# Optimization experiments

Measured on AMD Instinct MI355X. Metric: run time of the kernel, lower is better.

Reference implementation:

```python
import jax, jax.numpy as jnp
import numpy as np
from jax import lax

FACTOR = 2
FIR = (1.0, 3.0, 3.0, 1.0)


def _fir_kernel():
    k1 = jnp.array(FIR, dtype=jnp.float32)
    k = jnp.outer(k1, k1)
    k = k / jnp.sum(k)
    return k * (FACTOR ** 2)  # gain=1, factor=2 -> x4


def _upfirdn2d(x, kernel, up, down, pad):
    # x: [N, C, H, W]; kernel: [kh, kw]; faithful to upfirdn2d_native:
    # upsample by zero-insertion (lhs_dilation), pad, convolve with flipped
    # kernel (F.conv2d is correlation of flipped kernel == true convolution),
    # then downsample by striding. lax.conv_general_dilated is correlation,
    # so pass the flipped kernel.
    C = x.shape[1]
    kflip = kernel[::-1, ::-1]
    w = jnp.tile(kflip[None, None], (C, 1, 1, 1))  # depthwise [C,1,kh,kw]
    return lax.conv_general_dilated(
        x, w,
        window_strides=(down, down),
        padding=[(pad[0], pad[1]), (pad[0], pad[1])],
        lhs_dilation=(up, up),
        feature_group_count=C,
        dimension_numbers=("NCHW", "OIHW", "NCHW"),
    )


def setup_inputs() -> dict:
    key = jax.random.key(0)
    k1, k2, k3 = jax.random.split(key, 3)
    N, C, H, W = 8, 256, 64, 64
    outC = 256
    hidden_states = jax.random.normal(k1, (N, C, H, W), dtype=jnp.float32)
    weight = jax.random.normal(k2, (outC, C, 3, 3), dtype=jnp.float32) * 0.05
    bias = jax.random.normal(k3, (outC,), dtype=jnp.float32)
    return {"hidden_states": hidden_states, "weight": weight, "bias": bias}


def reference(hidden_states, weight, bias):
    # FirUpsample2D.forward with use_conv=True, fir_kernel=(1,3,3,1), factor=2.
    k = _fir_kernel()  # [4, 4]
    convH, convW = weight.shape[2], weight.shape[3]
    pad_value = k.shape[0] - FACTOR - (convW - 1)  # = 0 here

    # The torch code flips+channel-swaps the weight then calls conv_transpose2d
    # (which itself flips and channel-swaps); the two cancel, so the net op is
    # plain cross-correlation of the ORIGINAL weight over the factor-dilated
    # input with (kH-1) padding on each side (output_padding == 0).
    x = lax.conv_general_dilated(
        hidden_states, weight,
        window_strides=(1, 1),
        padding=[(convH - 1, convH - 1), (convW - 1, convW - 1)],
        lhs_dilation=(FACTOR, FACTOR),
        dimension_numbers=("NCHW", "OIHW", "NCHW"),
    )  # [N, outC, (H-1)*2+3, (W-1)*2+3]

    out = _upfirdn2d(
        x, k, up=1, down=1,
        pad=((pad_value + 1) // 2 + FACTOR - 1, pad_value // 2 + 1),
    )  # [N, outC, 2H, 2W]

    return out + bias[None, :, None, None]
```

## Files before the change

### kernel.cpp

```cpp
#include <hip/hip_runtime.h>
#include <cstdint>
#include <cstddef>

typedef _Float16 f16;
typedef _Float16 f16x8 __attribute__((ext_vector_type(8)));
typedef float f32x4 __attribute__((ext_vector_type(4)));

#define AS1 __attribute__((address_space(1)))
#define AS3 __attribute__((address_space(3)))

__device__ __forceinline__ void gl_lds16(const void* g, void* l) {
  __builtin_amdgcn_global_load_lds((AS1 void*)g, (AS3 void*)l, 16u, 0, 0u);
}

__constant__ float c_tab[2][3][3] = {
  {{0.75f, 0.25f, 0.00f}, {0.25f, 0.75f, 0.75f}, {0.00f, 0.00f, 0.25f}},
  {{0.25f, 0.00f, 0.00f}, {0.75f, 0.75f, 0.25f}, {0.00f, 0.25f, 0.75f}}
};

__global__ __launch_bounds__(256) void prep_k(const float* __restrict__ W,
                                              const float* __restrict__ In,
                                              f16* __restrict__ Et,
                                              f16* __restrict__ Ah) {
  const int b = blockIdx.x;
  const int tid = threadIdx.x;
  if (b < 256) {
    const int oc = b;
    const int ic = tid;
    const int c = ic >> 5, icl = ic & 31;
    float w[9];
    const float* wp = W + ((size_t)oc * 256 + ic) * 9;
#pragma unroll
    for (int t = 0; t < 9; ++t) w[t] = wp[t];
#pragma unroll
    for (int py = 0; py < 2; ++py)
#pragma unroll
      for (int px = 0; px < 2; ++px) {
        const int jj = oc * 4 + py * 2 + px;
#pragma unroll
        for (int ay = 0; ay < 3; ++ay)
#pragma unroll
          for (int ax = 0; ax < 3; ++ax) {
            float s = 0.f;
#pragma unroll
            for (int iy = 0; iy < 3; ++iy)
#pragma unroll
              for (int ix = 0; ix < 3; ++ix)
                s += w[iy * 3 + ix] * c_tab[py][ay][iy] * c_tab[px][ax][ix];
            Et[((size_t)(((c * 3 + ay) * 3 + ax) * 1024 + jj)) * 32 + icl] = (f16)s;
          }
      }
  } else {
    const int bid2 = b - 256;
    const int icc = bid2 & 7;
    const int v = bid2 >> 3;
    const int n = v / 66;
    const int yp = v - n * 66;
    const int ic0 = icc * 32;
    const int icl = tid & 31, x8 = tid >> 5;
    f16* rowbase = Ah + ((size_t)(n * 66 + yp) * 66) * 256 + ic0;
    if (yp == 0 || yp == 65) {
#pragma unroll
      for (int i = 0; i < 9; ++i) {
        const int xp = i * 8 + x8;
        if (xp < 66) rowbase[(size_t)xp * 256 + icl] = (f16)0.f;
      }
    } else {
      const int y = yp - 1;
      __shared__ float tile[32][65];
      const int xl = tid & 63, icl4 = tid >> 6;
      const float* src = In + (((size_t)(n * 256 + ic0)) * 64 + y) * 64;
#pragma unroll
      for (int i = 0; i < 8; ++i) {
        const int icl_ = i * 4 + icl4;
        tile[icl_][xl] = src[(size_t)icl_ * 4096 + xl];
      }
      __syncthreads();
      f16* dst = rowbase + 256;
#pragma unroll
      for (int i = 0; i < 8; ++i) {
        const int x = i * 8 + x8;
        dst[(size_t)x * 256 + icl] = (f16)tile[icl][x];
      }
      if (x8 == 0) {
        rowbase[icl] = (f16)0.f;
        rowbase[(size_t)65 * 256 + icl] = (f16)0.f;
      }
    }
  }
}

__global__ __launch_bounds__(256) void gemm_k(const f16* __restrict__ Ah,
                                              const f16* __restrict__ Et,
                                              const float* __restrict__ bias,
                                              float* __restrict__ out) {
  __shared__ __align__(256) f16 lA[2][4224];
  __shared__ __align__(256) f16 lB[2][12288];
  const int tid = threadIdx.x;
  const int wave = tid >> 6;
  const int lane = tid & 63;
  const int bid = blockIdx.x;
  const int nt = bid & 7;
  const int mt = bid >> 3;
  const int m0 = mt * 128;
  const int jj0 = nt * 128;
  const int n = m0 >> 12;
  const int y0 = (m0 >> 6) & 63;

  const int hig = (lane & 3) ^ ((lane >> 3) & 3);
  int goA[2];
#pragma unroll
  for (int i = 0; i < 2; ++i) {
    const int s = wave * 2 + i;
    const int u = s * 16 + (lane >> 2);
    const int row = (u >= 66) ? 1 : 0;
    const int x = u - 66 * row;
    goA[i] = ((row * 66 + x) * 256 + hig * 8) * 2;
  }
  const int goAt = ((66 + 62 + wave) * 256 + (((lane ^ (wave >> 1)) & 3)) * 8) * 2;
  int goB[6];
#pragma unroll
  for (int j = 0; j < 6; ++j) {
    const int t = wave + 4 * j;
    const int ax = t >> 3, sub = t & 7;
    goB[j] = (ax * 32768 + (sub * 16 + (lane >> 2)) * 32 + hig * 8) * 2;
  }
  char* const lAb = (char*)lA;
  char* const lBb = (char*)lB;

  const int wm = wave >> 1, wn = wave & 1;
  const int lr = lane & 15;
  const int hi16 = (lane >> 4) * 16;
  int rdA[4][3];
#pragma unroll
  for (int mi = 0; mi < 4; ++mi)
#pragma unroll
    for (int ax = 0; ax < 3; ++ax) {
      const int o = wm * 4224 + (lr + mi * 16 + ax) * 64 + hi16;
      rdA[mi][ax] = o ^ (((o >> 7) & 3) << 4);
    }
  int rdB[4][3];
#pragma unroll
  for (int ni = 0; ni < 4; ++ni)
#pragma unroll
    for (int ax = 0; ax < 3; ++ax) {
      const int o = (wn * 64 + lr) * 64 + hi16 + ax * 8192 + ni * 1024;
      rdB[ni][ax] = o ^ (((o >> 7) & 3) << 4);
    }

  const char* const aN = (const char*)Ah + (size_t)(n * 66 + y0) * 33792;
  const char* const bE = (const char*)Et + (size_t)jj0 * 64;

  const f32x4 vzero = {0.f, 0.f, 0.f, 0.f};
  f32x4 acc[4][4];
#pragma unroll
  for (int i = 0; i < 4; ++i)
#pragma unroll
    for (int j = 0; j < 4; ++j) acc[i][j] = vzero;

  {
    gl_lds16(aN + goA[0], lAb + (wave * 2 + 0) * 1024);
    gl_lds16(aN + goA[1], lAb + (wave * 2 + 1) * 1024);
    if (lane < 4) gl_lds16(aN + goAt, lAb + 8192 + wave * 64);
#pragma unroll
    for (int j = 0; j < 6; ++j) gl_lds16(bE + goB[j], lBb + (wave + 4 * j) * 1024);
  }

  const char* aPn = aN + 33792;
  const char* bPn = bE + 196608;
  int ayn = 1;

#pragma unroll 1
  for (int t = 0; t < 24; ++t) {
    const int p = t & 1;

    if (t < 23) {
      char* dA = lAb + (p ^ 1) * 8448;
      char* dB = lBb + (p ^ 1) * 24576;
      gl_lds16(aPn + goA[0], dA + (wave * 2 + 0) * 1024);
      gl_lds16(aPn + goA[1], dA + (wave * 2 + 1) * 1024);
      if (lane < 4) gl_lds16(aPn + goAt, dA + 8192 + wave * 64);
#pragma unroll
      for (int j = 0; j < 6; ++j) gl_lds16(bPn + goB[j], dB + (wave + 4 * j) * 1024);
      bPn += 196608;
      if (ayn == 2) { aPn -= 67520; ayn = 0; }
      else          { aPn += 33792; ++ayn; }
      asm volatile("s_waitcnt vmcnt(9)" ::: "memory");
    } else {
      asm volatile("s_waitcnt vmcnt(0)" ::: "memory");
    }
    __builtin_amdgcn_s_barrier();
    __builtin_amdgcn_sched_barrier(0);

    const char* sA = lAb + p * 8448;
    const char* sB = lBb + p * 24576;
    f16x8 af[3][4], bf[3][4];
#pragma unroll
    for (int ax = 0; ax < 3; ++ax) {
#pragma unroll
      for (int mi = 0; mi < 4; ++mi) af[ax][mi] = *(const f16x8*)(sA + rdA[mi][ax]);
#pragma unroll
      for (int ni = 0; ni < 4; ++ni) bf[ax][ni] = *(const f16x8*)(sB + rdB[ni][ax]);
    }
    asm volatile("s_waitcnt lgkmcnt(0)" ::: "memory");
    __builtin_amdgcn_sched_barrier(0);
    __builtin_amdgcn_s_barrier();

#pragma unroll
    for (int ax = 0; ax < 3; ++ax)
#pragma unroll
      for (int mi = 0; mi < 4; ++mi)
#pragma unroll
        for (int ni = 0; ni < 4; ++ni)
          acc[mi][ni] = __builtin_amdgcn_mfma_f32_16x16x32_f16(af[ax][mi], bf[ax][ni],
                                                               acc[mi][ni], 0, 0, 0);
  }

  const int yw = y0 + wm;
#pragma unroll
  for (int ni = 0; ni < 4; ++ni) {
    const int jj = jj0 + wn * 64 + ni * 16 + lr;
    const int oc = jj >> 2;
    const int py = (jj >> 1) & 1, px = jj & 1;
    const float bv = bias[oc];
    const int oy = 2 * yw + py;
    float* orow = out + ((size_t)(n * 256 + oc) * 128 + oy) * 128;
#pragma unroll
    for (int mi = 0; mi < 4; ++mi) {
      const int xb = mi * 16 + ((lane >> 4) << 2);
#pragma unroll
      for (int v = 0; v < 4; ++v) {
        orow[2 * (xb + v) + px] = acc[mi][ni][v] + bv;
      }
    }
  }
}

__global__ __launch_bounds__(256) void fallback_k(const float* __restrict__ In,
                                                  const float* __restrict__ W,
                                                  const float* __restrict__ bias,
                                                  float* __restrict__ out) {
  const size_t idx = (size_t)blockIdx.x * 256 + threadIdx.x;
  const int ox = (int)(idx & 127), oy = (int)((idx >> 7) & 127);
  const int oc = (int)((idx >> 14) & 255);
  const int n = (int)(idx >> 22);
  const int px = ox & 1, py = oy & 1;
  const int x = ox >> 1, y = oy >> 1;
  float cy[3][3], cx[3][3];
#pragma unroll
  for (int a = 0; a < 3; ++a)
#pragma unroll
    for (int i = 0; i < 3; ++i) {
      cy[a][i] = c_tab[py][a][i];
      cx[a][i] = c_tab[px][a][i];
    }
  float acc = 0.f;
  const float* wbase = W + (size_t)oc * 2304;
  for (int ic = 0; ic < 256; ++ic) {
    const float* ib = In + (((size_t)(n * 256 + ic)) * 64 + y) * 64 + x;
    float pin[3][3];
#pragma unroll
    for (int ay = 0; ay < 3; ++ay) {
      const int yy = y + ay - 1;
#pragma unroll
      for (int ax = 0; ax < 3; ++ax) {
        const int xx = x + ax - 1;
        pin[ay][ax] = (yy >= 0 && yy < 64 && xx >= 0 && xx < 64)
                          ? ib[(ay - 1) * 64 + (ax - 1)] : 0.f;
      }
    }
    const float* w = wbase + ic * 9;
    float U[3][3];
#pragma unroll
    for (int ay = 0; ay < 3; ++ay)
#pragma unroll
      for (int ix = 0; ix < 3; ++ix)
        U[ay][ix] = cx[0][ix] * pin[ay][0] + cx[1][ix] * pin[ay][1] + cx[2][ix] * pin[ay][2];
#pragma unroll
    for (int iy = 0; iy < 3; ++iy)
#pragma unroll
      for (int ix = 0; ix < 3; ++ix) {
        const float V = cy[0][iy] * U[0][ix] + cy[1][iy] * U[1][ix] + cy[2][iy] * U[2][ix];
        acc += w[iy * 3 + ix] * V;
      }
  }
  out[idx] = acc + bias[oc];
}

extern "C" void kernel_launch(void* const* d_in, const int* in_sizes, int n_in,
                              void* d_out, int out_size, void* d_ws, size_t ws_size,
                              hipStream_t stream) {
  const float* In = (const float*)d_in[0];
  const float* W = (const float*)d_in[1];
  const float* bias = (const float*)d_in[2];
  float* out = (float*)d_out;

  const size_t E_BYTES = (size_t)1024 * 2304 * 2;
  const size_t A_BYTES = (size_t)8 * 66 * 66 * 256 * 2;

  if (ws_size >= E_BYTES + A_BYTES) {
    f16* Et = (f16*)d_ws;
    f16* Ah = (f16*)((char*)d_ws + E_BYTES);
    prep_k<<<256 + 4224, 256, 0, stream>>>(W, In, Et, Ah);
    gemm_k<<<2048, 256, 0, stream>>>(Ah, Et, bias, out);
  } else {
    fallback_k<<<131072, 256, 0, stream>>>(In, W, bias, out);
  }
}
```

Baseline: 337.7 us.

## Enlarge GEMM tile to 256x256 with 512 threads and interleaved prefetch

Restructures the implicit-GEMM kernel from 128x128 tiles with 4 waves to 256x256 tiles with 8 waves, doubling LDS buffers and per-wave accumulators (8x4 MFMA tiles). The global-to-LDS prefetch for the next K-step is now issued inside the first ax sub-step, and LDS fragment loads are split per ax and interleaved with MFMA under raised wave priority. Block indices are remapped so consecutive blocks share the same M rows across N tiles, improving L2 reuse. The larger tile increases arithmetic intensity but raises register and LDS pressure (about 100KB LDS per block) and adds more barriers per iteration.

```diff
diff --git a/kernel.cpp b/kernel.cpp
--- a/kernel.cpp
+++ b/kernel.cpp
@@ -90,20 +90,20 @@
   }
 }
 
-__global__ __launch_bounds__(256) void gemm_k(const f16* __restrict__ Ah,
-                                              const f16* __restrict__ Et,
-                                              const float* __restrict__ bias,
-                                              float* __restrict__ out) {
-  __shared__ __align__(256) f16 lA[2][4224];
-  __shared__ __align__(256) f16 lB[2][12288];
+__global__ __launch_bounds__(512, 2) void gemm_k(const f16* __restrict__ Ah,
+                                                 const f16* __restrict__ Et,
+                                                 const float* __restrict__ bias,
+                                                 float* __restrict__ out) {
+  __shared__ __align__(256) f16 lA[2][8448];
+  __shared__ __align__(256) f16 lB[2][24576];
   const int tid = threadIdx.x;
   const int wave = tid >> 6;
   const int lane = tid & 63;
-  const int bid = blockIdx.x;
-  const int nt = bid & 7;
-  const int mt = bid >> 3;
-  const int m0 = mt * 128;
-  const int jj0 = nt * 128;
+  const int bid = (blockIdx.x & 7) * 64 + (blockIdx.x >> 3);
+  const int nt = bid & 3;
+  const int mt = bid >> 2;
+  const int m0 = mt * 256;
+  const int jj0 = nt * 256;
   const int n = m0 >> 12;
   const int y0 = (m0 >> 6) & 63;
 
@@ -113,121 +113,121 @@
   for (int i = 0; i < 2; ++i) {
     const int s = wave * 2 + i;
     const int u = s * 16 + (lane >> 2);
-    const int row = (u >= 66) ? 1 : 0;
-    const int x = u - 66 * row;
-    goA[i] = ((row * 66 + x) * 256 + hig * 8) * 2;
-  }
-  const int goAt = ((66 + 62 + wave) * 256 + (((lane ^ (wave >> 1)) & 3)) * 8) * 2;
+    const int r = u / 66;
+    const int xi = u - r * 66;
+    goA[i] = r * 33792 + xi * 512 + hig * 16;
+  }
+  const int goAt = 3 * 33792 + (58 + wave) * 512 + ((lane ^ (wave >> 1)) & 3) * 16;
   int goB[6];
 #pragma unroll
   for (int j = 0; j < 6; ++j) {
-    const int t = wave + 4 * j;
-    const int ax = t >> 3, sub = t & 7;
-    goB[j] = (ax * 32768 + (sub * 16 + (lane >> 2)) * 32 + hig * 8) * 2;
+    const int t = wave + 8 * j;
+    const int ax = t >> 4, jsl = t & 15;
+    goB[j] = ax * 65536 + (jsl * 16 + (lane >> 2)) * 64 + hig * 16;
   }
   char* const lAb = (char*)lA;
   char* const lBb = (char*)lB;
 
-  const int wm = wave >> 1, wn = wave & 1;
+  const int wm = wave >> 2, wn = wave & 3;
   const int lr = lane & 15;
   const int hi16 = (lane >> 4) * 16;
-  int rdA[4][3];
-#pragma unroll
-  for (int mi = 0; mi < 4; ++mi)
-#pragma unroll
-    for (int ax = 0; ax < 3; ++ax) {
-      const int o = wm * 4224 + (lr + mi * 16 + ax) * 64 + hi16;
-      rdA[mi][ax] = o ^ (((o >> 7) & 3) << 4);
-    }
-  int rdB[4][3];
-#pragma unroll
-  for (int ni = 0; ni < 4; ++ni)
-#pragma unroll
-    for (int ax = 0; ax < 3; ++ax) {
-      const int o = (wn * 64 + lr) * 64 + hi16 + ax * 8192 + ni * 1024;
-      rdB[ni][ax] = o ^ (((o >> 7) & 3) << 4);
-    }
-
-  const char* const aN = (const char*)Ah + (size_t)(n * 66 + y0) * 33792;
+  int rdA0[8];
+#pragma unroll
+  for (int mi = 0; mi < 8; ++mi)
+    rdA0[mi] = ((wm * 2 + (mi >> 2)) * 66 + (mi & 3) * 16 + lr) * 64 + hi16;
+  int rdBs[4];
+#pragma unroll
+  for (int ni = 0; ni < 4; ++ni) {
+    const int o = (wn * 64 + ni * 16 + lr) * 64 + hi16;
+    rdBs[ni] = o ^ (((o >> 7) & 3) << 4);
+  }
+
+  const char* const aBase = (const char*)Ah + ((size_t)(n * 66) + y0) * 33792;
   const char* const bE = (const char*)Et + (size_t)jj0 * 64;
 
   const f32x4 vzero = {0.f, 0.f, 0.f, 0.f};
-  f32x4 acc[4][4];
-#pragma unroll
-  for (int i = 0; i < 4; ++i)
+  f32x4 acc[8][4];
+#pragma unroll
+  for (int i = 0; i < 8; ++i)
 #pragma unroll
     for (int j = 0; j < 4; ++j) acc[i][j] = vzero;
 
   {
-    gl_lds16(aN + goA[0], lAb + (wave * 2 + 0) * 1024);
-    gl_lds16(aN + goA[1], lAb + (wave * 2 + 1) * 1024);
-    if (lane < 4) gl_lds16(aN + goAt, lAb + 8192 + wave * 64);
-#pragma unroll
-    for (int j = 0; j < 6; ++j) gl_lds16(bE + goB[j], lBb + (wave + 4 * j) * 1024);
-  }
-
-  const char* aPn = aN + 33792;
+    gl_lds16(aBase + goA[0], lAb + (wave * 2 + 0) * 1024);
+    gl_lds16(aBase + goA[1], lAb + (wave * 2 + 1) * 1024);
+    if (lane < 4) gl_lds16(aBase + goAt, lAb + 16384 + wave * 64);
+#pragma unroll
+    for (int j = 0; j < 6; ++j) gl_lds16(bE + goB[j], lBb + (wave + 8 * j) * 1024);
+  }
+  asm volatile("s_waitcnt vmcnt(0)" ::: "memory");
+  __builtin_amdgcn_s_barrier();
+
+  const char* aPn = aBase + 33792;
   const char* bPn = bE + 196608;
   int ayn = 1;
 
 #pragma unroll 1
   for (int t = 0; t < 24; ++t) {
     const int p = t & 1;
-
-    if (t < 23) {
-      char* dA = lAb + (p ^ 1) * 8448;
-      char* dB = lBb + (p ^ 1) * 24576;
-      gl_lds16(aPn + goA[0], dA + (wave * 2 + 0) * 1024);
-      gl_lds16(aPn + goA[1], dA + (wave * 2 + 1) * 1024);
-      if (lane < 4) gl_lds16(aPn + goAt, dA + 8192 + wave * 64);
-#pragma unroll
-      for (int j = 0; j < 6; ++j) gl_lds16(bPn + goB[j], dB + (wave + 4 * j) * 1024);
-      bPn += 196608;
-      if (ayn == 2) { aPn -= 67520; ayn = 0; }
-      else          { aPn += 33792; ++ayn; }
-      asm volatile("s_waitcnt vmcnt(9)" ::: "memory");
-    } else {
-      asm volatile("s_waitcnt vmcnt(0)" ::: "memory");
-    }
-    __builtin_amdgcn_s_barrier();
-    __builtin_amdgcn_sched_barrier(0);
-
-    const char* sA = lAb + p * 8448;
-    const char* sB = lBb + p * 24576;
-    f16x8 af[3][4], bf[3][4];
+    const char* sA = lAb + p * 16896;
+    const char* sB = lBb + p * 49152;
+
 #pragma unroll
     for (int ax = 0; ax < 3; ++ax) {
-#pragma unroll
-      for (int mi = 0; mi < 4; ++mi) af[ax][mi] = *(const f16x8*)(sA + rdA[mi][ax]);
-#pragma unroll
-      for (int ni = 0; ni < 4; ++ni) bf[ax][ni] = *(const f16x8*)(sB + rdB[ni][ax]);
-    }
-    asm volatile("s_waitcnt lgkmcnt(0)" ::: "memory");
-    __builtin_amdgcn_sched_barrier(0);
-    __builtin_amdgcn_s_barrier();
-
-#pragma unroll
-    for (int ax = 0; ax < 3; ++ax)
-#pragma unroll
-      for (int mi = 0; mi < 4; ++mi)
+      f16x8 af[8], bf[4];
+#pragma unroll
+      for (int mi = 0; mi < 8; ++mi) {
+        const int oa = rdA0[mi] + ax * 64;
+        const int sw = oa ^ (((oa >> 7) & 3) << 4);
+        af[mi] = *(const f16x8*)(sA + sw);
+      }
+#pragma unroll
+      for (int ni = 0; ni < 4; ++ni)
+        bf[ni] = *(const f16x8*)(sB + ax * 16384 + rdBs[ni]);
+
+      if (ax == 0 && t < 23) {
+        char* dA = lAb + (p ^ 1) * 16896;
+        char* dB = lBb + (p ^ 1) * 49152;
+        gl_lds16(aPn + goA[0], dA + (wave * 2 + 0) * 1024);
+        gl_lds16(aPn + goA[1], dA + (wave * 2 + 1) * 1024);
+        if (lane < 4) gl_lds16(aPn + goAt, dA + 16384 + wave * 64);
+#pragma unroll
+        for (int j = 0; j < 6; ++j) gl_lds16(bPn + goB[j], dB + (wave + 8 * j) * 1024);
+        bPn += 196608;
+        if (ayn == 2) { aPn -= 67520; ayn = 0; }
+        else          { aPn += 33792; ++ayn; }
+      }
+
+      __builtin_amdgcn_s_barrier();
+      asm volatile("s_waitcnt lgkmcnt(0)" ::: "memory");
+      __builtin_amdgcn_sched_barrier(0);
+
+      __builtin_amdgcn_s_setprio(1);
+#pragma unroll
+      for (int mi = 0; mi < 8; ++mi)
 #pragma unroll
         for (int ni = 0; ni < 4; ++ni)
-          acc[mi][ni] = __builtin_amdgcn_mfma_f32_16x16x32_f16(af[ax][mi], bf[ax][ni],
+          acc[mi][ni] = __builtin_amdgcn_mfma_f32_16x16x32_f16(af[mi], bf[ni],
                                                                acc[mi][ni], 0, 0, 0);
-  }
-
-  const int yw = y0 + wm;
+      __builtin_amdgcn_s_setprio(0);
+
+      if (ax == 2 && t < 23) asm volatile("s_waitcnt vmcnt(0)" ::: "memory");
+      __builtin_amdgcn_s_barrier();
+    }
+  }
+
 #pragma unroll
   for (int ni = 0; ni < 4; ++ni) {
     const int jj = jj0 + wn * 64 + ni * 16 + lr;
     const int oc = jj >> 2;
     const int py = (jj >> 1) & 1, px = jj & 1;
     const float bv = bias[oc];
-    const int oy = 2 * yw + py;
-    float* orow = out + ((size_t)(n * 256 + oc) * 128 + oy) * 128;
-#pragma unroll
-    for (int mi = 0; mi < 4; ++mi) {
-      const int xb = mi * 16 + ((lane >> 4) << 2);
+#pragma unroll
+    for (int mi = 0; mi < 8; ++mi) {
+      const int y = y0 + wm * 2 + (mi >> 2);
+      const int oy = 2 * y + py;
+      const int xb = (mi & 3) * 16 + ((lane >> 4) << 2);
+      float* orow = out + ((size_t)(n * 256 + oc) * 128 + oy) * 128;
 #pragma unroll
       for (int v = 0; v < 4; ++v) {
         orow[2 * (xb + v) + px] = acc[mi][ni][v] + bv;
@@ -302,7 +302,7 @@
     f16* Et = (f16*)d_ws;
     f16* Ah = (f16*)((char*)d_ws + E_BYTES);
     prep_k<<<256 + 4224, 256, 0, stream>>>(W, In, Et, Ah);
-    gemm_k<<<2048, 256, 0, stream>>>(Ah, Et, bias, out);
+    gemm_k<<<512, 512, 0, stream>>>(Ah, Et, bias, out);
   } else {
     fallback_k<<<131072, 256, 0, stream>>>(In, W, bias, out);
   }
```

After: 322.5 us. 1.05x faster.
